# Optimization experiments

Measured on AMD Instinct MI355X. Metric: run time of the kernel, lower is better.

## Reference

```python
import math
import jax, jax.numpy as jnp
import numpy as np

N = 4096        # nodes
D = 256         # input_dim
H = 8           # n_heads
HD = D // H     # head_dim
E = 131072      # edges (avg degree 32)
LEAKY_ALPHA = 0.2  # tf.nn.leaky_relu default


def setup_inputs() -> dict:
    key = jax.random.key(0)
    ks = jax.random.split(key, 8)
    inputs = jax.random.normal(ks[0], (N, D), dtype=jnp.float32)
    src = jax.random.randint(ks[1], (E,), 0, N, dtype=jnp.int64)
    dst = jax.random.randint(ks[2], (E,), 0, N, dtype=jnp.int64)
    s = 1.0 / np.sqrt(D).astype(np.float32)
    WQ = jax.random.normal(ks[3], (D, D), dtype=jnp.float32) * s
    WK = jax.random.normal(ks[4], (D, D), dtype=jnp.float32) * s
    WV = jax.random.normal(ks[5], (D, D), dtype=jnp.float32) * s
    Wc = jax.random.normal(ks[6], (D, D), dtype=jnp.float32) * s
    bc = jnp.zeros((D,), dtype=jnp.float32)
    return {"inputs": inputs, "src": src, "dst": dst,
            "WQ": WQ, "WK": WK, "WV": WV, "Wc": Wc, "bc": bc}


def reference(inputs, src, dst, WQ, WK, WV, Wc, bc):
    n, d = inputs.shape
    scale = max(1.0 / math.sqrt(d), 1e-6)
    Q = inputs @ WQ   # [n, d]
    K = inputs @ WK
    V = inputs @ WV
    # Original computes (Q_h K_h^T) @ A with A[src, dst] = 1.
    # Equivalently S[i, j] = Q_h[i] . (sum_{(m, j) in E} K_h[m]) = Q_h @ K2_h^T,
    # where K2 = segment_sum of K rows by edge destination (avoids dense A).
    K2 = jax.ops.segment_sum(K[src], dst, num_segments=n)  # [n, d]
    outs = []
    for h in range(H):  # fixed small head loop, mirrors original per-head loop
        sl = slice(h * HD, (h + 1) * HD)
        S = (Q[:, sl] @ K2[:, sl].T) * scale          # [n, n]
        P = jax.nn.softmax(S, axis=1)
        outs.append(P @ V[:, sl])                     # [n, HD]
    attn = jnp.concatenate(outs, axis=1)              # [n, d]
    h = inputs + attn                                 # residual (no BN at inference)
    h1 = jax.nn.leaky_relu(h @ Wc + bc, negative_slope=LEAKY_ALPHA)
    return h + h1
```

## Files before the change

kernel.cpp:

```cpp
#include <hip/hip_runtime.h>
#include <hip/hip_bf16.h>
#include <math.h>

#define DIM 256
#define HDIM 32
#define NN 4096
#define NM (NN * DIM)
#define PREF 0.09016844005555896f
#define LEAKY 0.2f
#define BCAP 128

typedef __attribute__((ext_vector_type(8))) short short8;
typedef __attribute__((ext_vector_type(16))) float f32x16;

#if __has_builtin(__builtin_amdgcn_exp2f)
#define EXP2(x) __builtin_amdgcn_exp2f(x)
#else
#define EXP2(x) exp2f(x)
#endif

static __device__ __forceinline__ unsigned bfbits(float x) {
  unsigned u = __float_as_uint(x);
  return (u + 0x7fffu + ((u >> 16) & 1u)) >> 16;
}
static __device__ __forceinline__ float bf2f(unsigned short b) {
  return __uint_as_float(((unsigned)b) << 16);
}
static __device__ __forceinline__ unsigned pk_bf16(float lo, float hi) {
  __hip_bfloat162 t = __float22bfloat162_rn(make_float2(lo, hi));
  return *(unsigned*)&t;
}

__global__ __launch_bounds__(256) void convert_w(
    const float* __restrict__ W0, const float* __restrict__ W1,
    const float* __restrict__ W2, const float* __restrict__ W3,
    unsigned short* __restrict__ Wtb, int* __restrict__ cnt) {
  const int tid = threadIdx.x;
  if (blockIdx.y == 0) cnt[blockIdx.x * 256 + tid] = 0;
  __shared__ float tile[64][68];
  const int wsel = blockIdx.y;
  const float* W = wsel == 0 ? W0 : (wsel == 1 ? W1 : (wsel == 2 ? W2 : W3));
  const float scale = wsel == 0 ? PREF : 1.f;
  const int kb = (blockIdx.x & 3) * 64, nb = (blockIdx.x >> 2) * 64;
#pragma unroll
  for (int i = 0; i < 4; ++i) {
    int idx = i * 256 + tid;
    int kr = idx >> 4, ns = idx & 15;
    float4 v = *(const float4*)&W[(kb + kr) * DIM + nb + ns * 4];
    tile[kr][ns * 4 + 0] = v.x; tile[kr][ns * 4 + 1] = v.y;
    tile[kr][ns * 4 + 2] = v.z; tile[kr][ns * 4 + 3] = v.w;
  }
  __syncthreads();
  unsigned short* o = Wtb + wsel * 65536;
#pragma unroll
  for (int i = 0; i < 2; ++i) {
    int idx = i * 256 + tid;
    int nr = idx >> 3, kslot = idx & 7;
    short8 v;
#pragma unroll
    for (int j = 0; j < 8; ++j)
      ((unsigned short*)&v)[j] = (unsigned short)bfbits(tile[kslot * 8 + j][nr] * scale);
    *(short8*)&o[(nb + nr) * DIM + kb + kslot * 8] = v;
  }
}

__global__ __launch_bounds__(256) void gemm_fill(
    const float* __restrict__ inp, const unsigned short* __restrict__ Wtb,
    const int* __restrict__ src, const int* __restrict__ dst, int E,
    int* __restrict__ cnt, int* __restrict__ esrc,
    unsigned short* __restrict__ Qb, unsigned short* __restrict__ Kb,
    unsigned short* __restrict__ Vtb) {
  __shared__ __align__(16) short sA[64 * 256];
  __shared__ __align__(16) short sB[64 * 256];
  const int tid = threadIdx.x;
  const int b = blockIdx.x;
  if (b >= 256) {
    int e = (b - 256) * 256 + tid;
    if (e < E) {
      int d = dst[e];
      int p = atomicAdd(&cnt[d], 1);
      if (p < BCAP) esrc[d * BCAP + p] = src[e];
    }
    return;
  }
  const int m0 = (b & 63) * 64;
  const int n0 = (b >> 6) * 64;
#pragma unroll
  for (int i = 0; i < 16; ++i) {
    int idx = i * 256 + tid;
    int row = idx >> 6, slot = idx & 63;
    float4 v = *(const float4*)&inp[(m0 + row) * DIM + slot * 4];
    uint2 pk = make_uint2(pk_bf16(v.x, v.y), pk_bf16(v.z, v.w));
    int byte = (slot * 8) ^ ((row & 15) << 4);
    *(uint2*)((char*)sA + row * 512 + byte) = pk;
  }
  const int kl = tid & 31, hi = (tid & 63) >> 5, w = tid >> 6;
  const int rw = (w >> 1) * 32, cw = (w & 1) * 32;
  const int arow = rw + kl, brow = cw + kl;
  const int axor = (arow & 15) << 4, bxor = (brow & 15) << 4;
  const char* apA = (const char*)sA + arow * 512;
  const char* apB = (const char*)sB + brow * 512;

#pragma unroll 1
  for (int wsel = 0; wsel < 3; ++wsel) {
    const unsigned short* Wt = Wtb + wsel * 65536;
    __syncthreads();
#pragma unroll
    for (int i = 0; i < 8; ++i) {
      int idx = i * 256 + tid;
      int row = idx >> 5, slot = idx & 31;
      short8 v = *(const short8*)&Wt[(n0 + row) * DIM + slot * 8];
      int byte = (slot * 16) ^ ((row & 15) << 4);
      *(short8*)((char*)sB + row * 512 + byte) = v;
    }
    __syncthreads();
    f32x16 acc;
#pragma unroll
    for (int r = 0; r < 16; ++r) acc[r] = 0.f;
#pragma unroll
    for (int ks = 0; ks < 16; ++ks) {
      int cb = ks * 32 + hi * 16;
      short8 a = *(const short8*)(apA + (cb ^ axor));
      short8 bfr = *(const short8*)(apB + (cb ^ bxor));
      acc = __builtin_amdgcn_mfma_f32_32x32x16_bf16(a, bfr, acc, 0, 0, 0);
    }
    if (wsel < 2) {
      unsigned short* C = wsel == 0 ? Qb : Kb;
#pragma unroll
      for (int r = 0; r < 16; ++r) {
        int mrow = (r & 3) + 8 * (r >> 2) + 4 * hi;
        C[(m0 + rw + mrow) * DIM + n0 + cw + kl] = (unsigned short)bfbits(acc[r]);
      }
    } else {
      __syncthreads();
      unsigned short* tile = (unsigned short*)sB;
#pragma unroll
      for (int r = 0; r < 16; ++r) {
        int mrow = (r & 3) + 8 * (r >> 2) + 4 * hi;
        tile[(rw + mrow) * 72 + cw + kl] = (unsigned short)bfbits(acc[r]);
      }
      __syncthreads();
#pragma unroll
      for (int i = 0; i < 2; ++i) {
        int idx = i * 256 + tid;
        int drow = idx >> 3, nslot = idx & 7;
        short8 v;
#pragma unroll
        for (int j = 0; j < 8; ++j)
          ((unsigned short*)&v)[j] = tile[(nslot * 8 + j) * 72 + drow];
        *(short8*)&Vtb[(n0 + drow) * NN + m0 + nslot * 8] = v;
      }
    }
  }
}

__global__ __launch_bounds__(256) void gather_k2(
    const unsigned short* __restrict__ Kb, const int* __restrict__ cnt,
    const int* __restrict__ esrc, unsigned short* __restrict__ K2b) {
  int w = threadIdx.x >> 6, lane = threadIdx.x & 63;
  int d = blockIdx.x * 4 + w;
  int n = cnt[d]; n = n > BCAP ? BCAP : n;
  const int* eb = esrc + d * BCAP;
  float a0 = 0, a1 = 0, a2 = 0, a3 = 0;
  int j = 0;
  for (; j + 4 <= n; j += 4) {
    int s0 = eb[j], s1 = eb[j + 1], s2 = eb[j + 2], s3 = eb[j + 3];
    ushort4 k0 = *(const ushort4*)&Kb[s0 * DIM + lane * 4];
    ushort4 k1 = *(const ushort4*)&Kb[s1 * DIM + lane * 4];
    ushort4 k2 = *(const ushort4*)&Kb[s2 * DIM + lane * 4];
    ushort4 k3 = *(const ushort4*)&Kb[s3 * DIM + lane * 4];
    a0 += bf2f(k0.x) + bf2f(k1.x) + bf2f(k2.x) + bf2f(k3.x);
    a1 += bf2f(k0.y) + bf2f(k1.y) + bf2f(k2.y) + bf2f(k3.y);
    a2 += bf2f(k0.z) + bf2f(k1.z) + bf2f(k2.z) + bf2f(k3.z);
    a3 += bf2f(k0.w) + bf2f(k1.w) + bf2f(k2.w) + bf2f(k3.w);
  }
  for (; j < n; ++j) {
    int s = eb[j];
    ushort4 kv = *(const ushort4*)&Kb[s * DIM + lane * 4];
    a0 += bf2f(kv.x); a1 += bf2f(kv.y); a2 += bf2f(kv.z); a3 += bf2f(kv.w);
  }
  ushort4 o;
  o.x = bfbits(a0); o.y = bfbits(a1); o.z = bfbits(a2); o.w = bfbits(a3);
  *(ushort4*)&K2b[d * DIM + lane * 4] = o;
}

static __device__ __forceinline__ void compute_tile64(
    const short* __restrict__ lk, const short* __restrict__ lv, int kl, int hi,
    short8 qf0, short8 qf1, const f32x16& zc, f32x16& o, float& lsum) {
#pragma unroll
  for (int sub = 0; sub < 2; ++sub) {
    const int base = sub * 32;
    short8 a0 = *(const short8*)&lk[(base + kl) * 40 + hi * 8];
    short8 a1 = *(const short8*)&lk[(base + kl) * 40 + 16 + hi * 8];
    __builtin_amdgcn_s_setprio(1);
    f32x16 c = __builtin_amdgcn_mfma_f32_32x32x16_bf16(a0, qf0, zc, 0, 0, 0);
    c = __builtin_amdgcn_mfma_f32_32x32x16_bf16(a1, qf1, c, 0, 0, 0);
    __builtin_amdgcn_s_setprio(0);
    float p[16];
#pragma unroll
    for (int r = 0; r < 16; ++r) p[r] = EXP2(c[r]);
    {
      float t0 = (p[0] + p[1]) + (p[2] + p[3]);
      float t1 = (p[4] + p[5]) + (p[6] + p[7]);
      float t2 = (p[8] + p[9]) + (p[10] + p[11]);
      float t3 = (p[12] + p[13]) + (p[14] + p[15]);
      lsum += (t0 + t1) + (t2 + t3);
    }
    unsigned X0 = pk_bf16(p[0], p[1]);
    unsigned Y0 = pk_bf16(p[2], p[3]);
    unsigned Z0 = pk_bf16(p[4], p[5]);
    unsigned W0 = pk_bf16(p[6], p[7]);
    asm volatile("v_permlane32_swap_b32 %0, %1" : "+v"(X0), "+v"(Z0));
    asm volatile("v_permlane32_swap_b32 %0, %1" : "+v"(Y0), "+v"(W0));
    unsigned X1 = pk_bf16(p[8], p[9]);
    unsigned Y1 = pk_bf16(p[10], p[11]);
    unsigned Z1 = pk_bf16(p[12], p[13]);
    unsigned W1 = pk_bf16(p[14], p[15]);
    asm volatile("v_permlane32_swap_b32 %0, %1" : "+v"(X1), "+v"(Z1));
    asm volatile("v_permlane32_swap_b32 %0, %1" : "+v"(Y1), "+v"(W1));
    short8 pb0, pb1;
    ((unsigned*)&pb0)[0] = X0; ((unsigned*)&pb0)[1] = Y0;
    ((unsigned*)&pb0)[2] = Z0; ((unsigned*)&pb0)[3] = W0;
    ((unsigned*)&pb1)[0] = X1; ((unsigned*)&pb1)[1] = Y1;
    ((unsigned*)&pb1)[2] = Z1; ((unsigned*)&pb1)[3] = W1;
    short8 va0 = *(const short8*)&lv[kl * 72 + base + hi * 8];
    short8 va1 = *(const short8*)&lv[kl * 72 + base + 16 + hi * 8];
    __builtin_amdgcn_s_setprio(1);
    o = __builtin_amdgcn_mfma_f32_32x32x16_bf16(va0, pb0, o, 0, 0, 0);
    o = __builtin_amdgcn_mfma_f32_32x32x16_bf16(va1, pb1, o, 0, 0, 0);
    __builtin_amdgcn_s_setprio(0);
  }
}

__global__ __launch_bounds__(512, 4) void attn_fused(
    const unsigned short* __restrict__ Qb, const unsigned short* __restrict__ K2b,
    const unsigned short* __restrict__ Vtb, const float* __restrict__ inp,
    unsigned short* __restrict__ Hbf) {
  __shared__ __align__(16) char smem[38912];
  __shared__ float lbuf[4][64];
  const int tid = threadIdx.x;
  const int lane = tid & 63;
  const int wid = tid >> 6;
  const int qw = wid & 1;
  const int zg = wid >> 1;
  const int kl = lane & 31;
  const int hi = lane >> 5;
  const int gtid = tid & 127;
  const int h = blockIdx.y, hc = h * HDIM;
  const int q_local = qw * 32 + kl;
  const int q = blockIdx.x * 64 + q_local;
  const int ks0 = zg * 1024;

  short* lk = (short*)smem + zg * 4864;
  short* lv = (short*)smem + zg * 4864 + 2560;

  const int kkey = gtid >> 1, kslot = gtid & 1;
  const int vdim = gtid >> 3, vslot = gtid & 7;
  const unsigned short* kg = &K2b[(ks0 + kkey) * DIM + hc + kslot * 16];
  const unsigned short* vg = &Vtb[(hc + vdim) * NN + ks0 + vslot * 8];
  short* lkw = lk + kkey * 40 + kslot * 16;
  short* lvw = lv + vdim * 72 + vslot * 8;

#define LOADKV(KR, VR)                                                      \
  do {                                                                      \
    KR[0] = *(const short8*)(kg);                                           \
    KR[1] = *(const short8*)(kg + 8);                                       \
    VR[0] = *(const short8*)(vg);                                           \
    VR[1] = *(const short8*)(vg + 16 * NN);                                 \
    kg += 64 * DIM; vg += 64;                                               \
  } while (0)
#define STOREKV(KR, VR)                                                     \
  do {                                                                      \
    *(short8*)(lkw) = KR[0];                                                \
    *(short8*)(lkw + 8) = KR[1];                                            \
    *(short8*)(lvw) = VR[0];                                                \
    *(short8*)(lvw + 16 * 72) = VR[1];                                      \
  } while (0)

  short8 qf0 = *(const short8*)&Qb[q * DIM + hc + hi * 8];
  short8 qf1 = *(const short8*)&Qb[q * DIM + hc + 16 + hi * 8];

  f32x16 zc;
#pragma unroll
  for (int r = 0; r < 16; ++r) zc[r] = 0.f;
  f32x16 o = zc;
  float lsum = 0.f;

  short8 kr[2], vr[2];
  LOADKV(kr, vr);
#pragma unroll 1
  for (int t = 0; t < 16; ++t) {
    __syncthreads();
    STOREKV(kr, vr);
    __syncthreads();
    if (t < 15) LOADKV(kr, vr);
    compute_tile64(lk, lv, kl, hi, qf0, qf1, zc, o, lsum);
  }
#undef LOADKV
#undef STOREKV

  float lt = lsum + __shfl_xor(lsum, 32);
  __syncthreads();
  float* mz = (float*)smem + zg * 2208;
#pragma unroll
  for (int r = 0; r < 16; ++r) {
    int d = (r & 3) + 8 * (r >> 2) + 4 * hi;
    mz[d * 69 + q_local] = o[r];
  }
  if (hi == 0) lbuf[zg][q_local] = lt;
  __syncthreads();
  {
    int ql = tid >> 3;
    int dg = (tid & 7) * 4;
    float s = (lbuf[0][ql] + lbuf[1][ql]) + (lbuf[2][ql] + lbuf[3][ql]);
    float inv = 1.f / s;
    const float* mb = (const float*)smem;
    float acc[4];
#pragma unroll
    for (int i = 0; i < 4; ++i) {
      int off = (dg + i) * 69 + ql;
      acc[i] = (mb[off] + mb[2208 + off]) + (mb[4416 + off] + mb[6624 + off]);
    }
    int qg = blockIdx.x * 64 + ql;
    float4 in4 = *(const float4*)&inp[qg * DIM + hc + dg];
    ushort4 hb;
    hb.x = bfbits(in4.x + acc[0] * inv);
    hb.y = bfbits(in4.y + acc[1] * inv);
    hb.z = bfbits(in4.z + acc[2] * inv);
    hb.w = bfbits(in4.w + acc[3] * inv);
    *(ushort4*)&Hbf[qg * DIM + hc + dg] = hb;
  }
}

__global__ __launch_bounds__(256) void gemm_final_mfma(
    const unsigned short* __restrict__ Hbf, const unsigned short* __restrict__ Wct,
    const float* __restrict__ bc, float* __restrict__ out) {
  __shared__ __align__(16) short sA[64 * 256];
  __shared__ __align__(16) short sB[64 * 256];
  const int tid = threadIdx.x;
  const int m0 = blockIdx.x * 64;
  const int n0 = blockIdx.y * 64;
#pragma unroll
  for (int i = 0; i < 8; ++i) {
    int idx = i * 256 + tid;
    int row = idx >> 5, slot = idx & 31;
    short8 v = *(const short8*)&Hbf[(m0 + row) * DIM + slot * 8];
    int byte = (slot * 16) ^ ((row & 15) << 4);
    *(short8*)((char*)sA + row * 512 + byte) = v;
  }
#pragma unroll
  for (int i = 0; i < 8; ++i) {
    int idx = i * 256 + tid;
    int row = idx >> 5, slot = idx & 31;
    short8 v = *(const short8*)&Wct[(n0 + row) * DIM + slot * 8];
    int byte = (slot * 16) ^ ((row & 15) << 4);
    *(short8*)((char*)sB + row * 512 + byte) = v;
  }
  __syncthreads();
  const int kl = tid & 31, hi = (tid & 63) >> 5, w = tid >> 6;
  const int rw = (w >> 1) * 32, cw = (w & 1) * 32;
  const int arow = rw + kl, brow = cw + kl;
  const int axor = (arow & 15) << 4, bxor = (brow & 15) << 4;
  const char* apA = (const char*)sA + arow * 512;
  const char* apB = (const char*)sB + brow * 512;
  f32x16 acc;
#pragma unroll
  for (int r = 0; r < 16; ++r) acc[r] = 0.f;
#pragma unroll
  for (int ks = 0; ks < 16; ++ks) {
    int cb = ks * 32 + hi * 16;
    short8 a = *(const short8*)(apA + (cb ^ axor));
    short8 b = *(const short8*)(apB + (cb ^ bxor));
    acc = __builtin_amdgcn_mfma_f32_32x32x16_bf16(a, b, acc, 0, 0, 0);
  }
#pragma unroll
  for (int r = 0; r < 16; ++r) {
    int mrow = (r & 3) + 8 * (r >> 2) + 4 * hi;
    int lrow = rw + mrow;
    int node = m0 + lrow, col = n0 + cw + kl;
    float x = acc[r] + bc[col];
    x = x > 0.f ? x : LEAKY * x;
    unsigned short hr = *(const unsigned short*)(
        (const char*)sA + lrow * 512 + ((col * 2) ^ ((lrow & 15) << 4)));
    out[node * DIM + col] = bf2f(hr) + x;
  }
}

extern "C" void kernel_launch(void* const* d_in, const int* in_sizes, int n_in,
                              void* d_out, int out_size, void* d_ws, size_t ws_size,
                              hipStream_t stream) {
  const float* inp = (const float*)d_in[0];
  const int* src   = (const int*)d_in[1];
  const int* dst   = (const int*)d_in[2];
  const float* WQ  = (const float*)d_in[3];
  const float* WK  = (const float*)d_in[4];
  const float* WV  = (const float*)d_in[5];
  const float* Wc  = (const float*)d_in[6];
  const float* bc  = (const float*)d_in[7];
  float* out = (float*)d_out;
  const int E = in_sizes[1];

  char* ws = (char*)d_ws;
  unsigned short* Qb  = (unsigned short*)(ws);
  unsigned short* Kb  = (unsigned short*)(ws + 2  * 1024 * 1024);
  unsigned short* Vtb = (unsigned short*)(ws + 4  * 1024 * 1024);
  unsigned short* K2b = (unsigned short*)(ws + 6  * 1024 * 1024);
  unsigned short* Wtb = (unsigned short*)(ws + 8  * 1024 * 1024);
  unsigned short* Hbf = (unsigned short*)(ws + 8 * 1024 * 1024 + 524288);
  int* cnt            = (int*)(ws + 10 * 1024 * 1024 + 524288);
  int* esrc           = (int*)(ws + 10 * 1024 * 1024 + 540672);

  const int fillBlocks = (E + 255) / 256;
  convert_w<<<dim3(16, 4), 256, 0, stream>>>(WQ, WK, WV, Wc, Wtb, cnt);
  gemm_fill<<<256 + fillBlocks, 256, 0, stream>>>(inp, Wtb, src, dst, E, cnt, esrc,
                                                  Qb, Kb, Vtb);
  gather_k2<<<NN / 4, 256, 0, stream>>>(Kb, cnt, esrc, K2b);
  attn_fused<<<dim3(64, 8), 512, 0, stream>>>(Qb, K2b, Vtb, inp, Hbf);
  gemm_final_mfma<<<dim3(64, 4), 256, 0, stream>>>(Hbf, Wtb + 3 * 65536, bc, out);
}
```

Before: 75.65 us.

## Split attention key range across two grid slices and merge partials in separate kernel

The attention kernel's key range is split in half along a new grid z dimension, doubling the block count from 512 to 1024. Each block writes unnormalized fp32 partial outputs and row sums to workspace. A new merge kernel combines the two halves, normalizes, adds the residual and writes the bf16 hidden state. This aims to fill more compute units on the MI355X, at the cost of an extra launch and about 8MB of fp32 partial traffic.

```diff
diff --git a/kernel.cpp b/kernel.cpp
--- a/kernel.cpp
+++ b/kernel.cpp
@@ -234,8 +234,8 @@
 
 __global__ __launch_bounds__(512, 4) void attn_fused(
     const unsigned short* __restrict__ Qb, const unsigned short* __restrict__ K2b,
-    const unsigned short* __restrict__ Vtb, const float* __restrict__ inp,
-    unsigned short* __restrict__ Hbf) {
+    const unsigned short* __restrict__ Vtb,
+    float* __restrict__ Op, float* __restrict__ Lp) {
   __shared__ __align__(16) char smem[38912];
   __shared__ float lbuf[4][64];
   const int tid = threadIdx.x;
@@ -247,9 +247,10 @@
   const int hi = lane >> 5;
   const int gtid = tid & 127;
   const int h = blockIdx.y, hc = h * HDIM;
+  const int zhalf = blockIdx.z;
   const int q_local = qw * 32 + kl;
   const int q = blockIdx.x * 64 + q_local;
-  const int ks0 = zg * 1024;
+  const int ks0 = zhalf * 2048 + zg * 512;
 
   short* lk = (short*)smem + zg * 4864;
   short* lv = (short*)smem + zg * 4864 + 2560;
@@ -289,11 +290,11 @@
   short8 kr[2], vr[2];
   LOADKV(kr, vr);
 #pragma unroll 1
-  for (int t = 0; t < 16; ++t) {
+  for (int t = 0; t < 8; ++t) {
     __syncthreads();
     STOREKV(kr, vr);
     __syncthreads();
-    if (t < 15) LOADKV(kr, vr);
+    if (t < 7) LOADKV(kr, vr);
     compute_tile64(lk, lv, kl, hi, qf0, qf1, zc, o, lsum);
   }
 #undef LOADKV
@@ -313,7 +314,6 @@
     int ql = tid >> 3;
     int dg = (tid & 7) * 4;
     float s = (lbuf[0][ql] + lbuf[1][ql]) + (lbuf[2][ql] + lbuf[3][ql]);
-    float inv = 1.f / s;
     const float* mb = (const float*)smem;
     float acc[4];
 #pragma unroll
@@ -322,14 +322,28 @@
       acc[i] = (mb[off] + mb[2208 + off]) + (mb[4416 + off] + mb[6624 + off]);
     }
     int qg = blockIdx.x * 64 + ql;
-    float4 in4 = *(const float4*)&inp[qg * DIM + hc + dg];
-    ushort4 hb;
-    hb.x = bfbits(in4.x + acc[0] * inv);
-    hb.y = bfbits(in4.y + acc[1] * inv);
-    hb.z = bfbits(in4.z + acc[2] * inv);
-    hb.w = bfbits(in4.w + acc[3] * inv);
-    *(ushort4*)&Hbf[qg * DIM + hc + dg] = hb;
-  }
+    *(float4*)&Op[zhalf * NM + qg * DIM + hc + dg] =
+        make_float4(acc[0], acc[1], acc[2], acc[3]);
+    if ((tid & 7) == 0) Lp[(zhalf * 8 + h) * NN + qg] = s;
+  }
+}
+
+__global__ __launch_bounds__(256) void merge_h(
+    const float* __restrict__ inp, const float* __restrict__ Op,
+    const float* __restrict__ Lp, unsigned short* __restrict__ Hbf) {
+  int i = (blockIdx.x * 256 + threadIdx.x) * 4;
+  int q = i >> 8;
+  int hh = (i & 255) >> 5;
+  float inv = 1.f / (Lp[hh * NN + q] + Lp[(8 + hh) * NN + q]);
+  float4 a = *(const float4*)&Op[i];
+  float4 b = *(const float4*)&Op[NM + i];
+  float4 in4 = *(const float4*)&inp[i];
+  ushort4 hb;
+  hb.x = bfbits(in4.x + (a.x + b.x) * inv);
+  hb.y = bfbits(in4.y + (a.y + b.y) * inv);
+  hb.z = bfbits(in4.z + (a.z + b.z) * inv);
+  hb.w = bfbits(in4.w + (a.w + b.w) * inv);
+  *(ushort4*)&Hbf[i] = hb;
 }
 
 __global__ __launch_bounds__(256) void gemm_final_mfma(
@@ -409,12 +423,15 @@
   unsigned short* Hbf = (unsigned short*)(ws + 8 * 1024 * 1024 + 524288);
   int* cnt            = (int*)(ws + 10 * 1024 * 1024 + 524288);
   int* esrc           = (int*)(ws + 10 * 1024 * 1024 + 540672);
+  float* Op           = (float*)(ws + 12 * 1024 * 1024 + 540672 + 16384);
+  float* Lp           = (float*)(ws + 20 * 1024 * 1024 + 540672 + 16384);
 
   const int fillBlocks = (E + 255) / 256;
   convert_w<<<dim3(16, 4), 256, 0, stream>>>(WQ, WK, WV, Wc, Wtb, cnt);
   gemm_fill<<<256 + fillBlocks, 256, 0, stream>>>(inp, Wtb, src, dst, E, cnt, esrc,
                                                   Qb, Kb, Vtb);
   gather_k2<<<NN / 4, 256, 0, stream>>>(Kb, cnt, esrc, K2b);
-  attn_fused<<<dim3(64, 8), 512, 0, stream>>>(Qb, K2b, Vtb, inp, Hbf);
+  attn_fused<<<dim3(64, 8, 2), 512, 0, stream>>>(Qb, K2b, Vtb, Op, Lp);
+  merge_h<<<NM / 1024, 256, 0, stream>>>(inp, Op, Lp, Hbf);
   gemm_final_mfma<<<dim3(64, 4), 256, 0, stream>>>(Hbf, Wtb + 3 * 65536, bc, out);
 }
```

New measurement: 79.75 us. +5.4%, slower.
